# Performance work log

Measured on AMD Instinct MI355X. Metric: run time of the kernel, lower is better.

## Reference

```python
import jax, jax.numpy as jnp
import numpy as np

N, E, D, H, L, G, C = 50000, 800000, 128, 128, 3, 128, 10
BN_EPS = 1e-5


def setup_inputs() -> dict:
    key = jax.random.key(0)
    ks = jax.random.split(key, 16)
    inp = {
        "x": jax.random.normal(ks[0], (N, D), dtype=jnp.float32),
        "node_centrality": jax.random.uniform(ks[1], (N,), dtype=jnp.float32),
        "edge_centrality": jax.random.uniform(ks[2], (E,), dtype=jnp.float32),
        # stacked per-layer MLP params (in == hidden so stackable)
        "W1": jax.random.normal(ks[3], (L, D, H), dtype=jnp.float32) * 0.05,
        "b1": jnp.zeros((L, H), dtype=jnp.float32),
        "g1": jnp.ones((L, H), dtype=jnp.float32),
        "be1": jnp.zeros((L, H), dtype=jnp.float32),
        "W2": jax.random.normal(ks[4], (L, H, H), dtype=jnp.float32) * 0.05,
        "b2": jnp.zeros((L, H), dtype=jnp.float32),
        "Wc": jax.random.normal(ks[5], (H, C), dtype=jnp.float32) * 0.05,
        "bc": jnp.zeros((C,), dtype=jnp.float32),
        "edge_index": jax.random.randint(ks[6], (2, E), 0, N, dtype=jnp.int64),
        "batch": jnp.sort(jax.random.randint(ks[7], (N,), 0, G, dtype=jnp.int64)),
    }
    return inp


def _gin_forward(x, node_centrality, edge_centrality, W1, b1, g1, be1, W2, b2, Wc, bc, edge_index, batch):
    src, dst = edge_index[0], edge_index[1]  # x_j = x[src], aggregate at dst
    ec = edge_centrality[:, None]
    nc = node_centrality[:, None]
    for l in range(L):
        # message: gather + scale by edge centrality; aggr='add': scatter-add
        msg = x[src] * ec                                      # [E, H]
        agg = jax.ops.segment_sum(msg, dst, num_segments=N)    # [N, H]
        h = agg * nc + x                                       # (1 + eps) * x_r, eps = 0
        # MLP([in, hidden, hidden]): Linear -> BatchNorm(train) -> ReLU -> Linear
        h = h @ W1[l] + b1[l]
        mu = h.mean(axis=0)
        var = h.var(axis=0)  # biased, matches BN training stats
        h = (h - mu) * jax.lax.rsqrt(var + BN_EPS) * g1[l] + be1[l]
        h = jax.nn.relu(h)
        h = h @ W2[l] + b2[l]
        x = jax.nn.relu(h)  # outer .relu() in GIN.forward
    # global mean pool over graphs
    sums = jax.ops.segment_sum(x, batch, num_segments=G)           # [G, H]
    cnt = jax.ops.segment_sum(jnp.ones((N,), x.dtype), batch, num_segments=G)
    pooled = sums / jnp.maximum(cnt, 1.0)[:, None]
    return pooled @ Wc + bc  # [G, C]


def reference(x, edge_index, batch, node_centrality, edge_centrality, W1, b1, g1, be1, W2, b2, Wc, bc):
    return _gin_forward(x, node_centrality, edge_centrality, W1, b1, g1, be1, W2, b2, Wc, bc, edge_index, batch)
```

## Files before the change

kernel.cpp:

```cpp
#include <hip/hip_runtime.h>

#define Nn 50000
#define Ee 800000
#define HD 128
#define Ll 3
#define Gg 128
#define Cc 10
#define BN_EPS 1e-5f
#define NBLK1 782
#define PPAD 800
#define NSCB 49

typedef __attribute__((ext_vector_type(8))) __bf16 bf16x8;
typedef __attribute__((ext_vector_type(4))) float f32x4;

__global__ void k_deg(const int* __restrict__ dst, int* __restrict__ deg) {
  int i = blockIdx.x * blockDim.x + threadIdx.x;
  int stride = gridDim.x * blockDim.x;
  for (int e = i; e < Ee; e += stride) atomicAdd(&deg[dst[e]], 1);
}

__global__ void k_scan1(const int* __restrict__ deg, int* __restrict__ offs,
                        int* __restrict__ bsum) {
  __shared__ int b0[1024], b1[1024];
  int tid = threadIdx.x;
  int i = blockIdx.x * 1024 + tid;
  int v = (i < Nn) ? deg[i] : 0;
  int* cur = b0; int* nxt = b1;
  cur[tid] = v;
  __syncthreads();
  for (int off = 1; off < 1024; off <<= 1) {
    int s = cur[tid] + ((tid >= off) ? cur[tid - off] : 0);
    nxt[tid] = s;
    __syncthreads();
    int* t = cur; cur = nxt; nxt = t;
  }
  if (i < Nn) offs[i] = cur[tid] - v;
  if (tid == 1023) bsum[blockIdx.x] = cur[1023];
}

__global__ void k_scan2(const int* __restrict__ bsum, int* __restrict__ carry) {
  int lane = threadIdx.x;
  int v = (lane < NSCB) ? bsum[lane] : 0;
  int s = v;
  for (int off = 1; off < 64; off <<= 1) {
    int t = __shfl_up(s, off, 64);
    if (lane >= off) s += t;
  }
  if (lane < NSCB) carry[lane] = s - v;
}

__global__ void k_scan3(const int* __restrict__ carry, int* __restrict__ offs,
                        int* __restrict__ cursor) {
  int i = blockIdx.x * 1024 + threadIdx.x;
  if (i < Nn) {
    int o = offs[i] + carry[blockIdx.x];
    offs[i] = o; cursor[i] = o;
  }
  if (i == 0) offs[Nn] = Ee;
}

__global__ void k_fill(const int* __restrict__ src, const int* __restrict__ dst,
                       const float* __restrict__ ec, int* __restrict__ cursor,
                       int2* __restrict__ epk) {
  int i = blockIdx.x * blockDim.x + threadIdx.x;
  int stride = gridDim.x * blockDim.x;
  for (int e = i; e < Ee; e += stride) {
    int d = dst[e];
    int p = atomicAdd(&cursor[d], 1);
    epk[p] = make_int2(src[e], __float_as_int(ec[e]));
  }
}

__global__ void k_wprep(const float* __restrict__ W1, const float* __restrict__ W2,
                        __bf16* __restrict__ wtHi, __bf16* __restrict__ wtLo) {
  int mat = blockIdx.x >> 3;
  int chunk = blockIdx.x & 7;
  const float* W = (mat < 3) ? (W1 + mat * 16384) : (W2 + (mat - 3) * 16384);
  __bf16* hi = wtHi + mat * 16384;
  __bf16* lo = wtLo + mat * 16384;
  for (int t = threadIdx.x; t < 2048; t += blockDim.x) {
    int idx = chunk * 2048 + t;
    int n = idx >> 7, k = idx & 127;
    float v = W[k * 128 + n];
    __bf16 h = (__bf16)v;
    hi[idx] = h;
    lo[idx] = (__bf16)(v - (float)h);
  }
}

__global__ void k_agg(const float* __restrict__ xin, const int* __restrict__ offs,
                      const int2* __restrict__ epk, float* __restrict__ agg) {
  int wid = threadIdx.x >> 6, lane = threadIdx.x & 63;
  int n = blockIdx.x * 4 + wid;
  if (n >= Nn) return;
  int beg = offs[n], end = offs[n + 1];
  const float2* x2 = (const float2*)xin;
  float2 a0 = make_float2(0.f, 0.f), a1 = make_float2(0.f, 0.f);
  float2 a2 = make_float2(0.f, 0.f), a3 = make_float2(0.f, 0.f);
  int j = beg;
  for (; j + 3 < end; j += 4) {
    int2 e0 = epk[j], e1 = epk[j + 1], e2 = epk[j + 2], e3 = epk[j + 3];
    float2 v0 = x2[e0.x * 64 + lane];
    float2 v1 = x2[e1.x * 64 + lane];
    float2 v2 = x2[e2.x * 64 + lane];
    float2 v3 = x2[e3.x * 64 + lane];
    float w0 = __int_as_float(e0.y), w1 = __int_as_float(e1.y);
    float w2 = __int_as_float(e2.y), w3 = __int_as_float(e3.y);
    a0.x = fmaf(v0.x, w0, a0.x); a0.y = fmaf(v0.y, w0, a0.y);
    a1.x = fmaf(v1.x, w1, a1.x); a1.y = fmaf(v1.y, w1, a1.y);
    a2.x = fmaf(v2.x, w2, a2.x); a2.y = fmaf(v2.y, w2, a2.y);
    a3.x = fmaf(v3.x, w3, a3.x); a3.y = fmaf(v3.y, w3, a3.y);
  }
  for (; j < end; ++j) {
    int2 e = epk[j];
    float2 v = x2[e.x * 64 + lane];
    float w = __int_as_float(e.y);
    a0.x = fmaf(v.x, w, a0.x); a0.y = fmaf(v.y, w, a0.y);
  }
  a0.x += a1.x + a2.x + a3.x;
  a0.y += a1.y + a2.y + a3.y;
  ((float2*)agg)[n * 64 + lane] = a0;
}

__device__ __forceinline__ void split8(const float* a, bf16x8& hi, bf16x8& lo) {
#pragma unroll
  for (int j = 0; j < 8; ++j) {
    float v = a[j];
    __bf16 h = (__bf16)v;
    hi[j] = h;
    lo[j] = (__bf16)(v - (float)h);
  }
}

__launch_bounds__(128)
__global__ void k_gemm1(const float* __restrict__ agg, const float* __restrict__ nc,
                        const float* __restrict__ xin,
                        const __bf16* __restrict__ wtHi, const __bf16* __restrict__ wtLo,
                        const float* __restrict__ bias, float* __restrict__ out,
                        float* __restrict__ partial) {
  int tid = threadIdx.x;
  int w = tid >> 6, l = tid & 63;
  int row0 = blockIdx.x * 64;
  int l15 = l & 15, lg = l >> 4;
  int colw = w * 64;
  int krow = lg * 8;

  f32x4 acc[4][4];
#pragma unroll
  for (int m = 0; m < 4; ++m)
#pragma unroll
    for (int n = 0; n < 4; ++n) acc[m][n] = (f32x4){0.f, 0.f, 0.f, 0.f};

  int rowA[4]; bool rv[4]; float ncv[4];
#pragma unroll
  for (int m = 0; m < 4; ++m) {
    rowA[m] = row0 + m * 16 + l15;
    rv[m] = rowA[m] < Nn;
    ncv[m] = rv[m] ? nc[rowA[m]] : 0.f;
  }

#pragma unroll
  for (int ks = 0; ks < 4; ++ks) {
    int k0 = ks * 32 + krow;
    bf16x8 aHi[4], aLo[4];
#pragma unroll
    for (int m = 0; m < 4; ++m) {
      float av[8];
      if (rv[m]) {
        const float* ap = agg + rowA[m] * 128 + k0;
        const float* xp = xin + rowA[m] * 128 + k0;
        f32x4 g0 = *(const f32x4*)ap, g1 = *(const f32x4*)(ap + 4);
        f32x4 x0 = *(const f32x4*)xp, x1 = *(const f32x4*)(xp + 4);
#pragma unroll
        for (int jj = 0; jj < 4; ++jj) {
          av[jj]     = fmaf(g0[jj], ncv[m], x0[jj]);
          av[4 + jj] = fmaf(g1[jj], ncv[m], x1[jj]);
        }
      } else {
#pragma unroll
        for (int jj = 0; jj < 8; ++jj) av[jj] = 0.f;
      }
      split8(av, aHi[m], aLo[m]);
    }
    bf16x8 bHi[4], bLo[4];
#pragma unroll
    for (int n = 0; n < 4; ++n) {
      int c = colw + n * 16 + l15;
      bHi[n] = *(const bf16x8*)(wtHi + c * 128 + k0);
      bLo[n] = *(const bf16x8*)(wtLo + c * 128 + k0);
    }
#pragma unroll
    for (int m = 0; m < 4; ++m)
#pragma unroll
      for (int n = 0; n < 4; ++n) {
        acc[m][n] = __builtin_amdgcn_mfma_f32_16x16x32_bf16(aHi[m], bHi[n], acc[m][n], 0, 0, 0);
        acc[m][n] = __builtin_amdgcn_mfma_f32_16x16x32_bf16(aLo[m], bHi[n], acc[m][n], 0, 0, 0);
        acc[m][n] = __builtin_amdgcn_mfma_f32_16x16x32_bf16(aHi[m], bLo[n], acc[m][n], 0, 0, 0);
      }
  }

  float s[4] = {0.f, 0.f, 0.f, 0.f}, q[4] = {0.f, 0.f, 0.f, 0.f};
#pragma unroll
  for (int n = 0; n < 4; ++n) {
    int c = colw + n * 16 + l15;
    float bv = bias[c];
#pragma unroll
    for (int m = 0; m < 4; ++m) {
      int rbase = row0 + m * 16 + lg * 4;
#pragma unroll
      for (int r = 0; r < 4; ++r) {
        int rr = rbase + r;
        if (rr < Nn) {
          float o = acc[m][n][r] + bv;
          out[rr * 128 + c] = o;
          s[n] += o; q[n] += o * o;
        }
      }
    }
  }
#pragma unroll
  for (int n = 0; n < 4; ++n) {
    s[n] += __shfl_xor(s[n], 16, 64); q[n] += __shfl_xor(q[n], 16, 64);
    s[n] += __shfl_xor(s[n], 32, 64); q[n] += __shfl_xor(q[n], 32, 64);
  }
  if (lg == 0) {
    int blk = blockIdx.x;
#pragma unroll
    for (int n = 0; n < 4; ++n) {
      int f = colw + n * 16 + l15;
      partial[f * PPAD + blk] = s[n];
      partial[(128 + f) * PPAD + blk] = q[n];
    }
  }
}

__global__ void k_bnfin(const float* __restrict__ partial,
                        const float* __restrict__ g1, const float* __restrict__ be1,
                        float* __restrict__ scaleA, float* __restrict__ shiftA) {
  __shared__ float ss[256], qq[256];
  int f = blockIdx.x, t = threadIdx.x;
  float s = 0.f, q = 0.f;
  for (int b = t; b < NBLK1; b += 256) {
    s += partial[f * PPAD + b];
    q += partial[(128 + f) * PPAD + b];
  }
  ss[t] = s; qq[t] = q;
  __syncthreads();
  for (int off = 128; off > 0; off >>= 1) {
    if (t < off) { ss[t] += ss[t + off]; qq[t] += qq[t + off]; }
    __syncthreads();
  }
  if (t == 0) {
    const float inv = 1.0f / (float)Nn;
    float mu = ss[0] * inv;
    float var = fmaxf(qq[0] * inv - mu * mu, 0.f);
    float rs = rsqrtf(var + BN_EPS);
    float sc = rs * g1[f];
    scaleA[f] = sc;
    shiftA[f] = be1[f] - mu * sc;
  }
}

__launch_bounds__(128)
__global__ void k_gemm2(const float* __restrict__ h1, const float* __restrict__ scaleA,
                        const float* __restrict__ shiftA,
                        const __bf16* __restrict__ wtHi, const __bf16* __restrict__ wtLo,
                        const float* __restrict__ bias, float* __restrict__ out) {
  int tid = threadIdx.x;
  int w = tid >> 6, l = tid & 63;
  int row0 = blockIdx.x * 64;
  int l15 = l & 15, lg = l >> 4;
  int colw = w * 64;
  int krow = lg * 8;

  f32x4 acc[4][4];
#pragma unroll
  for (int m = 0; m < 4; ++m)
#pragma unroll
    for (int n = 0; n < 4; ++n) acc[m][n] = (f32x4){0.f, 0.f, 0.f, 0.f};

  int rowA[4]; bool rv[4];
#pragma unroll
  for (int m = 0; m < 4; ++m) {
    rowA[m] = row0 + m * 16 + l15;
    rv[m] = rowA[m] < Nn;
  }

#pragma unroll
  for (int ks = 0; ks < 4; ++ks) {
    int k0 = ks * 32 + krow;
    f32x4 sc0 = *(const f32x4*)(scaleA + k0), sc1 = *(const f32x4*)(scaleA + k0 + 4);
    f32x4 sh0 = *(const f32x4*)(shiftA + k0), sh1 = *(const f32x4*)(shiftA + k0 + 4);
    bf16x8 aHi[4], aLo[4];
#pragma unroll
    for (int m = 0; m < 4; ++m) {
      float av[8];
      if (rv[m]) {
        const float* hp = h1 + rowA[m] * 128 + k0;
        f32x4 h0 = *(const f32x4*)hp, h1v = *(const f32x4*)(hp + 4);
#pragma unroll
        for (int jj = 0; jj < 4; ++jj) {
          av[jj]     = fmaxf(fmaf(h0[jj],  sc0[jj], sh0[jj]), 0.f);
          av[4 + jj] = fmaxf(fmaf(h1v[jj], sc1[jj], sh1[jj]), 0.f);
        }
      } else {
#pragma unroll
        for (int jj = 0; jj < 8; ++jj) av[jj] = 0.f;
      }
      split8(av, aHi[m], aLo[m]);
    }
    bf16x8 bHi[4], bLo[4];
#pragma unroll
    for (int n = 0; n < 4; ++n) {
      int c = colw + n * 16 + l15;
      bHi[n] = *(const bf16x8*)(wtHi + c * 128 + k0);
      bLo[n] = *(const bf16x8*)(wtLo + c * 128 + k0);
    }
#pragma unroll
    for (int m = 0; m < 4; ++m)
#pragma unroll
      for (int n = 0; n < 4; ++n) {
        acc[m][n] = __builtin_amdgcn_mfma_f32_16x16x32_bf16(aHi[m], bHi[n], acc[m][n], 0, 0, 0);
        acc[m][n] = __builtin_amdgcn_mfma_f32_16x16x32_bf16(aLo[m], bHi[n], acc[m][n], 0, 0, 0);
        acc[m][n] = __builtin_amdgcn_mfma_f32_16x16x32_bf16(aHi[m], bLo[n], acc[m][n], 0, 0, 0);
      }
  }

#pragma unroll
  for (int n = 0; n < 4; ++n) {
    int c = colw + n * 16 + l15;
    float bv = bias[c];
#pragma unroll
    for (int m = 0; m < 4; ++m) {
      int rbase = row0 + m * 16 + lg * 4;
#pragma unroll
      for (int r = 0; r < 4; ++r) {
        int rr = rbase + r;
        if (rr < Nn) out[rr * 128 + c] = fmaxf(acc[m][n][r] + bv, 0.f);
      }
    }
  }
}

#define PCH 64
__global__ void k_pool(const float* __restrict__ xin, const int* __restrict__ batch,
                       float* __restrict__ pooled, float* __restrict__ gcnt) {
  int wid = threadIdx.x >> 6, lane = threadIdx.x & 63;
  int w = blockIdx.x * 4 + wid;
  int n0 = w * PCH;
  if (n0 >= Nn) return;
  int n1 = (n0 + PCH < Nn) ? n0 + PCH : Nn;
  const float2* x2 = (const float2*)xin;
  float2 acc = make_float2(0.f, 0.f);
  int cur = batch[n0];
  int cnt = 0;
  for (int n = n0; n < n1; ++n) {
    int g = batch[n];
    if (g != cur) {
      atomicAdd(&pooled[cur * 128 + lane * 2 + 0], acc.x);
      atomicAdd(&pooled[cur * 128 + lane * 2 + 1], acc.y);
      if (lane == 0) atomicAdd(&gcnt[cur], (float)cnt);
      acc = make_float2(0.f, 0.f); cnt = 0; cur = g;
    }
    float2 v = x2[n * 64 + lane];
    acc.x += v.x; acc.y += v.y; ++cnt;
  }
  atomicAdd(&pooled[cur * 128 + lane * 2 + 0], acc.x);
  atomicAdd(&pooled[cur * 128 + lane * 2 + 1], acc.y);
  if (lane == 0) atomicAdd(&gcnt[cur], (float)cnt);
}

__global__ void k_head(const float* __restrict__ pooled, const float* __restrict__ gcnt,
                       const float* __restrict__ Wc, const float* __restrict__ bc,
                       float* __restrict__ out) {
  __shared__ float p[128];
  int g = blockIdx.x, tid = threadIdx.x;
  p[tid] = pooled[g * 128 + tid] / fmaxf(gcnt[g], 1.0f);
  __syncthreads();
  if (tid < Cc) {
    float acc = bc[tid];
    for (int k = 0; k < 128; ++k) acc = fmaf(p[k], Wc[k * Cc + tid], acc);
    out[g * Cc + tid] = acc;
  }
}

extern "C" void kernel_launch(void* const* d_in, const int* in_sizes, int n_in,
                              void* d_out, int out_size, void* d_ws, size_t ws_size,
                              hipStream_t stream) {
  const float* x    = (const float*)d_in[0];
  const float* ncn  = (const float*)d_in[1];
  const float* ecn  = (const float*)d_in[2];
  const float* W1   = (const float*)d_in[3];
  const float* b1   = (const float*)d_in[4];
  const float* g1   = (const float*)d_in[5];
  const float* be1  = (const float*)d_in[6];
  const float* W2   = (const float*)d_in[7];
  const float* b2   = (const float*)d_in[8];
  const float* Wc   = (const float*)d_in[9];
  const float* bc   = (const float*)d_in[10];
  const int*   ei   = (const int*)d_in[11];
  const int*   batch= (const int*)d_in[12];
  const int* src  = ei;
  const int* dstp = ei + Ee;

  float* fws = (float*)d_ws;
  float* bufA     = fws;
  float* bufB     = fws +  6400000;
  float* h1       = fws + 12800000;
  float* partial  = fws + 19200000;
  float* scaleA   = partial + 256 * PPAD;
  float* shiftA   = scaleA + 128;
  float* pooled   = shiftA + 128;
  float* gcnt     = pooled + Gg * 128;
  int*   ib       = (int*)(gcnt + 128);
  int*   deg      = ib;
  int*   offs     = deg + Nn;
  int*   cursor   = offs + Nn + 64;
  int*   bsum     = cursor + Nn;
  int*   carry    = bsum + 64;
  int2*  epk      = (int2*)(carry + 64);
  __bf16* wtHi    = (__bf16*)(epk + Ee);
  __bf16* wtLo    = wtHi + 6 * 16384;

  k_wprep<<<48, 256, 0, stream>>>(W1, W2, wtHi, wtLo);
  hipMemsetAsync(deg, 0, Nn * sizeof(int), stream);
  k_deg<<<1024, 256, 0, stream>>>(dstp, deg);
  k_scan1<<<NSCB, 1024, 0, stream>>>(deg, offs, bsum);
  k_scan2<<<1, 64, 0, stream>>>(bsum, carry);
  k_scan3<<<NSCB, 1024, 0, stream>>>(carry, offs, cursor);
  k_fill<<<1024, 256, 0, stream>>>(src, dstp, ecn, cursor, epk);

  const float* xin = x;
  for (int l = 0; l < Ll; ++l) {
    float* aggb = (l & 1) ? bufB : bufA;
    k_agg<<<(Nn + 3) / 4, 256, 0, stream>>>(xin, offs, epk, aggb);
    k_gemm1<<<NBLK1, 128, 0, stream>>>(aggb, ncn, xin,
                                       wtHi + l * 16384, wtLo + l * 16384,
                                       b1 + l * 128, h1, partial);
    k_bnfin<<<128, 256, 0, stream>>>(partial, g1 + l * 128, be1 + l * 128,
                                     scaleA, shiftA);
    k_gemm2<<<NBLK1, 128, 0, stream>>>(h1, scaleA, shiftA,
                                       wtHi + (3 + l) * 16384, wtLo + (3 + l) * 16384,
                                       b2 + l * 128, aggb);
    xin = aggb;
  }

  hipMemsetAsync(pooled, 0, (Gg * 128 + 128) * sizeof(float), stream);
  k_pool<<<(Nn + PCH * 4 - 1) / (PCH * 4), 256, 0, stream>>>(xin, batch, pooled, gcnt);
  k_head<<<Gg, 128, 0, stream>>>(pooled, gcnt, Wc, bc, (float*)d_out);
}
```

Measured before the change: 583.9 us.

## Gather bf16 node features and pack edges into 32-bit src/fp16 weight

After: 536.6 us. 1.09x faster.

```diff
diff --git a/kernel.cpp b/kernel.cpp
--- a/kernel.cpp
+++ b/kernel.cpp
@@ -1,4 +1,5 @@
 #include <hip/hip_runtime.h>
+#include <hip/hip_fp16.h>
 
 #define Nn 50000
 #define Ee 800000
@@ -12,12 +13,18 @@
 #define NSCB 49
 
 typedef __attribute__((ext_vector_type(8))) __bf16 bf16x8;
+typedef __attribute__((ext_vector_type(4))) __bf16 bf16x4;
 typedef __attribute__((ext_vector_type(4))) float f32x4;
 
 __global__ void k_deg(const int* __restrict__ dst, int* __restrict__ deg) {
   int i = blockIdx.x * blockDim.x + threadIdx.x;
-  int stride = gridDim.x * blockDim.x;
-  for (int e = i; e < Ee; e += stride) atomicAdd(&deg[dst[e]], 1);
+  int base = i * 4;
+  if (base >= Ee) return;
+#pragma unroll
+  for (int j = 0; j < 4; ++j) {
+    int e = base + j;
+    if (e < Ee) atomicAdd(&deg[dst[e]], 1);
+  }
 }
 
 __global__ void k_scan1(const int* __restrict__ deg, int* __restrict__ offs,
@@ -62,13 +69,38 @@
 
 __global__ void k_fill(const int* __restrict__ src, const int* __restrict__ dst,
                        const float* __restrict__ ec, int* __restrict__ cursor,
-                       int2* __restrict__ epk) {
+                       unsigned int* __restrict__ epk) {
+  int i = blockIdx.x * blockDim.x + threadIdx.x;
+  int base = i * 4;
+  if (base >= Ee) return;
+  int d[4], s[4], p[4]; unsigned short hb[4]; bool ok[4];
+#pragma unroll
+  for (int j = 0; j < 4; ++j) {
+    int e = base + j;
+    ok[j] = e < Ee;
+    if (ok[j]) {
+      d[j] = dst[e]; s[j] = src[e];
+      hb[j] = __half_as_ushort(__float2half(ec[e]));
+    }
+  }
+#pragma unroll
+  for (int j = 0; j < 4; ++j)
+    if (ok[j]) p[j] = atomicAdd(&cursor[d[j]], 1);
+#pragma unroll
+  for (int j = 0; j < 4; ++j)
+    if (ok[j]) epk[p[j]] = ((unsigned int)s[j] << 16) | hb[j];
+}
+
+__global__ void k_xcast(const float* __restrict__ x, __bf16* __restrict__ xb) {
   int i = blockIdx.x * blockDim.x + threadIdx.x;
   int stride = gridDim.x * blockDim.x;
-  for (int e = i; e < Ee; e += stride) {
-    int d = dst[e];
-    int p = atomicAdd(&cursor[d], 1);
-    epk[p] = make_int2(src[e], __float_as_int(ec[e]));
+  const int n4 = Nn * 32;
+  for (int t = i; t < n4; t += stride) {
+    f32x4 v = ((const f32x4*)x)[t];
+    bf16x4 b;
+#pragma unroll
+    for (int j = 0; j < 4; ++j) b[j] = (__bf16)v[j];
+    ((bf16x4*)xb)[t] = b;
   }
 }
 
@@ -89,38 +121,46 @@
   }
 }
 
-__global__ void k_agg(const float* __restrict__ xin, const int* __restrict__ offs,
-                      const int2* __restrict__ epk, float* __restrict__ agg) {
+__global__ void k_agg(const __bf16* __restrict__ xb, const int* __restrict__ offs,
+                      const unsigned int* __restrict__ epk, float* __restrict__ agg) {
   int wid = threadIdx.x >> 6, lane = threadIdx.x & 63;
   int n = blockIdx.x * 4 + wid;
   if (n >= Nn) return;
   int beg = offs[n], end = offs[n + 1];
-  const float2* x2 = (const float2*)xin;
-  float2 a0 = make_float2(0.f, 0.f), a1 = make_float2(0.f, 0.f);
-  float2 a2 = make_float2(0.f, 0.f), a3 = make_float2(0.f, 0.f);
+  const unsigned int* x2 = (const unsigned int*)xb;
+  float ax0 = 0.f, ay0 = 0.f, ax1 = 0.f, ay1 = 0.f;
+  float ax2 = 0.f, ay2 = 0.f, ax3 = 0.f, ay3 = 0.f;
   int j = beg;
   for (; j + 3 < end; j += 4) {
-    int2 e0 = epk[j], e1 = epk[j + 1], e2 = epk[j + 2], e3 = epk[j + 3];
-    float2 v0 = x2[e0.x * 64 + lane];
-    float2 v1 = x2[e1.x * 64 + lane];
-    float2 v2 = x2[e2.x * 64 + lane];
-    float2 v3 = x2[e3.x * 64 + lane];
-    float w0 = __int_as_float(e0.y), w1 = __int_as_float(e1.y);
-    float w2 = __int_as_float(e2.y), w3 = __int_as_float(e3.y);
-    a0.x = fmaf(v0.x, w0, a0.x); a0.y = fmaf(v0.y, w0, a0.y);
-    a1.x = fmaf(v1.x, w1, a1.x); a1.y = fmaf(v1.y, w1, a1.y);
-    a2.x = fmaf(v2.x, w2, a2.x); a2.y = fmaf(v2.y, w2, a2.y);
-    a3.x = fmaf(v3.x, w3, a3.x); a3.y = fmaf(v3.y, w3, a3.y);
+    unsigned int e0 = epk[j], e1 = epk[j + 1], e2 = epk[j + 2], e3 = epk[j + 3];
+    unsigned int v0 = x2[(e0 >> 16) * 64 + lane];
+    unsigned int v1 = x2[(e1 >> 16) * 64 + lane];
+    unsigned int v2 = x2[(e2 >> 16) * 64 + lane];
+    unsigned int v3 = x2[(e3 >> 16) * 64 + lane];
+    __half_raw h0, h1, h2, h3;
+    h0.x = (unsigned short)(e0 & 0xffffu); h1.x = (unsigned short)(e1 & 0xffffu);
+    h2.x = (unsigned short)(e2 & 0xffffu); h3.x = (unsigned short)(e3 & 0xffffu);
+    float w0 = __half2float(h0), w1 = __half2float(h1);
+    float w2 = __half2float(h2), w3 = __half2float(h3);
+    ax0 = fmaf(__uint_as_float(v0 << 16), w0, ax0);
+    ay0 = fmaf(__uint_as_float(v0 & 0xffff0000u), w0, ay0);
+    ax1 = fmaf(__uint_as_float(v1 << 16), w1, ax1);
+    ay1 = fmaf(__uint_as_float(v1 & 0xffff0000u), w1, ay1);
+    ax2 = fmaf(__uint_as_float(v2 << 16), w2, ax2);
+    ay2 = fmaf(__uint_as_float(v2 & 0xffff0000u), w2, ay2);
+    ax3 = fmaf(__uint_as_float(v3 << 16), w3, ax3);
+    ay3 = fmaf(__uint_as_float(v3 & 0xffff0000u), w3, ay3);
   }
   for (; j < end; ++j) {
-    int2 e = epk[j];
-    float2 v = x2[e.x * 64 + lane];
-    float w = __int_as_float(e.y);
-    a0.x = fmaf(v.x, w, a0.x); a0.y = fmaf(v.y, w, a0.y);
-  }
-  a0.x += a1.x + a2.x + a3.x;
-  a0.y += a1.y + a2.y + a3.y;
-  ((float2*)agg)[n * 64 + lane] = a0;
+    unsigned int e = epk[j];
+    unsigned int v = x2[(e >> 16) * 64 + lane];
+    __half_raw h; h.x = (unsigned short)(e & 0xffffu);
+    float w = __half2float(h);
+    ax0 = fmaf(__uint_as_float(v << 16), w, ax0);
+    ay0 = fmaf(__uint_as_float(v & 0xffff0000u), w, ay0);
+  }
+  float2 acc = make_float2(ax0 + ax1 + ax2 + ax3, ay0 + ay1 + ay2 + ay3);
+  ((float2*)agg)[n * 64 + lane] = acc;
 }
 
 __device__ __forceinline__ void split8(const float* a, bf16x8& hi, bf16x8& lo) {
@@ -266,7 +306,8 @@
 __global__ void k_gemm2(const float* __restrict__ h1, const float* __restrict__ scaleA,
                         const float* __restrict__ shiftA,
                         const __bf16* __restrict__ wtHi, const __bf16* __restrict__ wtLo,
-                        const float* __restrict__ bias, float* __restrict__ out) {
+                        const float* __restrict__ bias, float* __restrict__ out,
+                        __bf16* __restrict__ xbout) {
   int tid = threadIdx.x;
   int w = tid >> 6, l = tid & 63;
   int row0 = blockIdx.x * 64;
@@ -337,7 +378,11 @@
 #pragma unroll
       for (int r = 0; r < 4; ++r) {
         int rr = rbase + r;
-        if (rr < Nn) out[rr * 128 + c] = fmaxf(acc[m][n][r] + bv, 0.f);
+        if (rr < Nn) {
+          float o = fmaxf(acc[m][n][r] + bv, 0.f);
+          out[rr * 128 + c] = o;
+          xbout[rr * 128 + c] = (__bf16)o;
+        }
       }
     }
   }
@@ -419,22 +464,24 @@
   int*   cursor   = offs + Nn + 64;
   int*   bsum     = cursor + Nn;
   int*   carry    = bsum + 64;
-  int2*  epk      = (int2*)(carry + 64);
+  unsigned int* epk = (unsigned int*)(carry + 64);
   __bf16* wtHi    = (__bf16*)(epk + Ee);
   __bf16* wtLo    = wtHi + 6 * 16384;
+  __bf16* xb      = wtLo + 6 * 16384;
 
   k_wprep<<<48, 256, 0, stream>>>(W1, W2, wtHi, wtLo);
+  k_xcast<<<2048, 256, 0, stream>>>(x, xb);
   hipMemsetAsync(deg, 0, Nn * sizeof(int), stream);
-  k_deg<<<1024, 256, 0, stream>>>(dstp, deg);
+  k_deg<<<(Ee / 4 + 255) / 256, 256, 0, stream>>>(dstp, deg);
   k_scan1<<<NSCB, 1024, 0, stream>>>(deg, offs, bsum);
   k_scan2<<<1, 64, 0, stream>>>(bsum, carry);
   k_scan3<<<NSCB, 1024, 0, stream>>>(carry, offs, cursor);
-  k_fill<<<1024, 256, 0, stream>>>(src, dstp, ecn, cursor, epk);
+  k_fill<<<(Ee / 4 + 255) / 256, 256, 0, stream>>>(src, dstp, ecn, cursor, epk);
 
   const float* xin = x;
   for (int l = 0; l < Ll; ++l) {
     float* aggb = (l & 1) ? bufB : bufA;
-    k_agg<<<(Nn + 3) / 4, 256, 0, stream>>>(xin, offs, epk, aggb);
+    k_agg<<<(Nn + 3) / 4, 256, 0, stream>>>(xb, offs, epk, aggb);
     k_gemm1<<<NBLK1, 128, 0, stream>>>(aggb, ncn, xin,
                                        wtHi + l * 16384, wtLo + l * 16384,
                                        b1 + l * 128, h1, partial);
@@ -442,7 +489,7 @@
                                      scaleA, shiftA);
     k_gemm2<<<NBLK1, 128, 0, stream>>>(h1, scaleA, shiftA,
                                        wtHi + (3 + l) * 16384, wtLo + (3 + l) * 16384,
-                                       b2 + l * 128, aggb);
+                                       b2 + l * 128, aggb, xb);
     xin = aggb;
   }
 
```
